# Performance work log

Hardware: AMD Instinct MI355X
Metric: run time of the kernel (lower is better)

Reference implementation:

```python
import jax, jax.numpy as jnp
import numpy as np

PATCH_LEN = 25
RATIO = 0.1
B, C, T = 128, 128, 5000
NUM_PATCHES = T // PATCH_LEN          # 200
TOTAL_UNITS = C * NUM_PATCHES         # 25600
NUM_MASK = int(TOTAL_UNITS * RATIO)   # 2560


def setup_inputs() -> dict:
    key = jax.random.key(0)
    kx, kp = jax.random.split(key)
    x = jax.random.normal(kx, (B, C, T), dtype=jnp.float32)
    # torch.randperm(total_units)[:num_mask] -> unique unit indices
    idx = jax.random.permutation(kp, TOTAL_UNITS)[:NUM_MASK].astype(jnp.int32)
    return {"x": x, "idx": idx}


def reference(x, idx):
    # Fused mask-generate-and-multiply: one scatter + one elementwise multiply
    # instead of num_mask separate slice-assign kernels.
    Bx, Cx, Tx = x.shape
    num_patches = Tx // PATCH_LEN
    # unit mask over (C * num_patches): 0 at masked units, 1 elsewhere
    unit_mask = jnp.ones((Cx * num_patches,), dtype=x.dtype).at[idx].set(0.0)
    # expand each unit to its patch_len samples -> (C, T)
    mask = jnp.repeat(unit_mask.reshape(Cx, num_patches), PATCH_LEN, axis=1)
    return x * mask[None, :, :]
```

## Files before the change

kernel.cpp:

```cpp
#include <hip/hip_runtime.h>


#define PM_B 128
#define PM_C 128
#define PM_T 5000
#define PM_PATCH 25
#define PM_NP 200
#define PM_UNITS (PM_C * PM_NP)
#define PM_NMASK 2560
#define PM_F4_PER_ROW (PM_T / 4)
#define PM_F4_TOTAL (PM_B * PM_C * PM_F4_PER_ROW)

typedef float f32x4 __attribute__((ext_vector_type(4)));

__global__ void pm_scatter_mask(const int* __restrict__ idx, float* __restrict__ um) {
    int i = blockIdx.x * blockDim.x + threadIdx.x;
    if (i < PM_NMASK) um[idx[i]] = 1.0f;
}

__global__ __launch_bounds__(256) void pm_apply_mask(
    const f32x4* __restrict__ x,
    const float* __restrict__ um,
    f32x4* __restrict__ out)
{
    unsigned i = blockIdx.x * 256u + threadIdx.x;
    const unsigned stride = gridDim.x * 256u;
    for (; i < PM_F4_TOTAL; i += stride) {
        const unsigned row = i / PM_F4_PER_ROW;
        const unsigned t0  = (i - row * PM_F4_PER_ROW) * 4u;
        const float* __restrict__ um_c = um + (row & (PM_C - 1)) * PM_NP;

        f32x4 v = __builtin_nontemporal_load(x + i);

        const unsigned p0 = t0 / PM_PATCH;
        const unsigned p3 = (t0 + 3u) / PM_PATCH;
        const float m0 = 1.0f - um_c[p0];
        if (p0 == p3) {
            v *= m0;
        } else {
            const float m3 = 1.0f - um_c[p3];
            const unsigned boundary = p3 * PM_PATCH;
            v.x *= (t0 + 0u < boundary) ? m0 : m3;
            v.y *= (t0 + 1u < boundary) ? m0 : m3;
            v.z *= (t0 + 2u < boundary) ? m0 : m3;
            v.w *= (t0 + 3u < boundary) ? m0 : m3;
        }

        __builtin_nontemporal_store(v, out + i);
    }
}

extern "C" void kernel_launch(void* const* d_in, const int* in_sizes, int n_in,
                              void* d_out, int out_size, void* d_ws, size_t ws_size,
                              hipStream_t stream) {
    const float* x   = (const float*)d_in[0];
    const int*   idx = (const int*)d_in[1];
    float*       out = (float*)d_out;
    float*       um  = (float*)d_ws;

    (void)hipMemsetAsync(um, 0, PM_UNITS * sizeof(float), stream);
    pm_scatter_mask<<<(PM_NMASK + 255) / 256, 256, 0, stream>>>(idx, um);

    pm_apply_mask<<<2048, 256, 0, stream>>>(
        (const f32x4*)x, um, (f32x4*)out);
}
```

Baseline: 125.0 us.

## Fuse mask scatter into apply kernel using per-block shared-memory bitmask

Drops the memset and the separate scatter kernel. Each block now builds a 25600-bit mask in LDS with atomicOr over the 2560 indices, then applies it while the main loop handles two float4 elements per iteration. This removes two extra launches and the global mask reads. In exchange, every one of the 2048 blocks redoes the index scatter, which adds idx reads and LDS atomics before any streaming starts.

```diff
diff --git a/kernel.cpp b/kernel.cpp
--- a/kernel.cpp
+++ b/kernel.cpp
@@ -10,44 +10,63 @@
 #define PM_NMASK 2560
 #define PM_F4_PER_ROW (PM_T / 4)
 #define PM_F4_TOTAL (PM_B * PM_C * PM_F4_PER_ROW)
+#define PM_MWORDS (PM_UNITS / 32)
 
 typedef float f32x4 __attribute__((ext_vector_type(4)));
 
-__global__ void pm_scatter_mask(const int* __restrict__ idx, float* __restrict__ um) {
-    int i = blockIdx.x * blockDim.x + threadIdx.x;
-    if (i < PM_NMASK) um[idx[i]] = 1.0f;
+__device__ __forceinline__ void pm_process(
+    unsigned i, const f32x4* __restrict__ x, f32x4* __restrict__ out,
+    const unsigned* mbits)
+{
+    const unsigned row = i / PM_F4_PER_ROW;
+    const unsigned t0  = (i - row * PM_F4_PER_ROW) * 4u;
+    const unsigned cbase = (row & (PM_C - 1)) * PM_NP;
+
+    f32x4 v = __builtin_nontemporal_load(x + i);
+
+    const unsigned p0 = t0 / PM_PATCH;
+    const unsigned p3 = (t0 + 3u) / PM_PATCH;
+    const unsigned u0 = cbase + p0;
+    const float m0 = ((mbits[u0 >> 5] >> (u0 & 31u)) & 1u) ? 0.0f : 1.0f;
+    if (p0 == p3) {
+        v *= m0;
+    } else {
+        const unsigned u3 = cbase + p3;
+        const float m3 = ((mbits[u3 >> 5] >> (u3 & 31u)) & 1u) ? 0.0f : 1.0f;
+        const unsigned boundary = p3 * PM_PATCH;
+        v.x *= (t0 + 0u < boundary) ? m0 : m3;
+        v.y *= (t0 + 1u < boundary) ? m0 : m3;
+        v.z *= (t0 + 2u < boundary) ? m0 : m3;
+        v.w *= (t0 + 3u < boundary) ? m0 : m3;
+    }
+
+    __builtin_nontemporal_store(v, out + i);
 }
 
-__global__ __launch_bounds__(256) void pm_apply_mask(
+__global__ __launch_bounds__(256) void pm_fused(
     const f32x4* __restrict__ x,
-    const float* __restrict__ um,
+    const int* __restrict__ idx,
     f32x4* __restrict__ out)
 {
+    __shared__ unsigned mbits[PM_MWORDS];
+
+    for (unsigned w = threadIdx.x; w < PM_MWORDS; w += 256u)
+        mbits[w] = 0u;
+    __syncthreads();
+    for (unsigned j = threadIdx.x; j < PM_NMASK; j += 256u) {
+        const unsigned u = (unsigned)idx[j];
+        atomicOr(&mbits[u >> 5], 1u << (u & 31u));
+    }
+    __syncthreads();
+
     unsigned i = blockIdx.x * 256u + threadIdx.x;
     const unsigned stride = gridDim.x * 256u;
-    for (; i < PM_F4_TOTAL; i += stride) {
-        const unsigned row = i / PM_F4_PER_ROW;
-        const unsigned t0  = (i - row * PM_F4_PER_ROW) * 4u;
-        const float* __restrict__ um_c = um + (row & (PM_C - 1)) * PM_NP;
-
-        f32x4 v = __builtin_nontemporal_load(x + i);
-
-        const unsigned p0 = t0 / PM_PATCH;
-        const unsigned p3 = (t0 + 3u) / PM_PATCH;
-        const float m0 = 1.0f - um_c[p0];
-        if (p0 == p3) {
-            v *= m0;
-        } else {
-            const float m3 = 1.0f - um_c[p3];
-            const unsigned boundary = p3 * PM_PATCH;
-            v.x *= (t0 + 0u < boundary) ? m0 : m3;
-            v.y *= (t0 + 1u < boundary) ? m0 : m3;
-            v.z *= (t0 + 2u < boundary) ? m0 : m3;
-            v.w *= (t0 + 3u < boundary) ? m0 : m3;
-        }
-
-        __builtin_nontemporal_store(v, out + i);
+    for (; i + stride < PM_F4_TOTAL; i += 2u * stride) {
+        pm_process(i,          x, out, mbits);
+        pm_process(i + stride, x, out, mbits);
     }
+    if (i < PM_F4_TOTAL)
+        pm_process(i, x, out, mbits);
 }
 
 extern "C" void kernel_launch(void* const* d_in, const int* in_sizes, int n_in,
@@ -56,11 +75,7 @@
     const float* x   = (const float*)d_in[0];
     const int*   idx = (const int*)d_in[1];
     float*       out = (float*)d_out;
-    float*       um  = (float*)d_ws;
 
-    (void)hipMemsetAsync(um, 0, PM_UNITS * sizeof(float), stream);
-    pm_scatter_mask<<<(PM_NMASK + 255) / 256, 256, 0, stream>>>(idx, um);
-
-    pm_apply_mask<<<2048, 256, 0, stream>>>(
-        (const f32x4*)x, um, (f32x4*)out);
+    pm_fused<<<2048, 256, 0, stream>>>(
+        (const f32x4*)x, idx, (f32x4*)out);
 }
```

New measurement: 123.8 us. About the same (-1.0%).
